# Performance work log

Measured on AMD Instinct MI355X. Metric: run time of the kernel, lower is better.

The kernel has to match this reference:

```python
import jax, jax.numpy as jnp
import numpy as np

B, L, D, H = 2, 2048, 1024, 16
DK = D // H
DFF = 4 * D
EPS = 1e-5  # torch LayerNorm default


def setup_inputs() -> dict:
    key = jax.random.key(0)
    ks = jax.random.split(key, 12)
    w = lambda k, shp: (jax.random.normal(k, shp, jnp.float32) * 0.02)
    return {
        "x": jax.random.normal(ks[0], (B, L, D), jnp.float32),
        "y": jax.random.normal(ks[1], (B, L, D), jnp.float32),
        "Wq": w(ks[2], (D, D)), "bq": jnp.zeros((D,), jnp.float32),
        "Wk": w(ks[3], (D, D)), "bk": jnp.zeros((D,), jnp.float32),
        "Wv": w(ks[4], (D, D)), "bv": jnp.zeros((D,), jnp.float32),
        "Wo": w(ks[5], (D, D)), "bo": jnp.zeros((D,), jnp.float32),
        "W1": w(ks[6], (D, DFF)), "b1": jnp.zeros((DFF,), jnp.float32),
        "W2": w(ks[7], (DFF, D)), "b2": jnp.zeros((D,), jnp.float32),
        "ln1_w": jnp.ones((L, D), jnp.float32), "ln1_b": jnp.zeros((L, D), jnp.float32),
        "ln2_w": jnp.ones((L, D), jnp.float32), "ln2_b": jnp.zeros((L, D), jnp.float32),
    }


def _layernorm2d(t, w, b):
    # nn.LayerNorm(normalized_shape=[L, D]): normalize jointly over last two dims
    mu = jnp.mean(t, axis=(-2, -1), keepdims=True)
    var = jnp.mean((t - mu) ** 2, axis=(-2, -1), keepdims=True)
    return (t - mu) * jax.lax.rsqrt(var + EPS) * w + b


def _attention(q_in, kv_in, Wq, bq, Wk, bk, Wv, bv, Wo, bo):
    split = lambda t: t.reshape(B, L, H, DK).transpose(0, 2, 1, 3)  # [B,H,L,DK]
    q = split(q_in @ Wq + bq)
    k = split(kv_in @ Wk + bk)
    v = split(kv_in @ Wv + bv)
    scores = jnp.einsum("bhqd,bhkd->bhqk", q, k) / (DK ** 0.5)
    # NOTE: original applies torch.tril to SCORES (zeroes upper triangle,
    # NOT -inf), so future positions still contribute exp(0)=1 in softmax.
    scores = jnp.tril(scores)
    p_attn = jax.nn.softmax(scores, axis=-1)
    out = jnp.einsum("bhqk,bhkd->bhqd", p_attn, v)
    out = out.transpose(0, 2, 1, 3).reshape(B, L, D)
    return out @ Wo + bo


def reference(x, y, Wq, bq, Wk, bk, Wv, bv, Wo, bo, W1, b1, W2, b2,
              ln1_w, ln1_b, ln2_w, ln2_b):
    # sublayer 0: pre-norm y, attention(query=x, key=value=norm(y)), residual
    y1 = y + _attention(x, _layernorm2d(y, ln1_w, ln1_b),
                        Wq, bq, Wk, bk, Wv, bv, Wo, bo)
    # sublayer 1: pre-norm, FFN (dropout inactive in eval), residual
    h = jax.nn.relu(_layernorm2d(y1, ln2_w, ln2_b) @ W1 + b1)
    return y1 + h @ W2 + b2
```

## Files before the change

### kernel.cpp

```cpp
#include <hip/hip_runtime.h>
#include <math.h>

#define B 2
#define L 2048
#define D 1024
#define H 16
#define DK 64
#define DFF 4096
#define EPS 1e-5f

typedef short short8 __attribute__((ext_vector_type(8)));
typedef short short4v __attribute__((ext_vector_type(4)));
typedef float float4v __attribute__((ext_vector_type(4)));
typedef unsigned int u32;

__device__ inline short f2bf(float f) {
    unsigned u = __builtin_bit_cast(unsigned, f);
    u += 0x7fffu + ((u >> 16) & 1u);
    return (short)(u >> 16);
}

__device__ inline float bf2f(short s) {
    unsigned u = ((unsigned)(unsigned short)s) << 16;
    return __builtin_bit_cast(float, u);
}

#define GLOAD_LDS16(gp, lp)                                                  \
    __builtin_amdgcn_global_load_lds(                                        \
        (const __attribute__((address_space(1))) u32*)(const void*)(gp),     \
        (__attribute__((address_space(3))) u32*)(void*)(lp), 16, 0, 0)

__device__ inline void xcd_remap(int& bx, int& by) {
    const int nbx = gridDim.x, nby = gridDim.y;
    const int orig = blockIdx.x + nbx * blockIdx.y;
    const int k = orig & 7, j = orig >> 3;
    const int nyc = nby >> 3;
    bx = j % nbx;
    by = k * nyc + j / nbx;
}


__global__ __launch_bounds__(256) void red_partial(const float* __restrict__ X,
                                                   float* __restrict__ part) {
    int b = blockIdx.y;
    const float4* p = (const float4*)(X + (size_t)b * L * D);
    float s = 0.f, ss = 0.f;
    for (int idx = blockIdx.x * 256 + threadIdx.x; idx < L * D / 4; idx += 256 * 256) {
        float4 v = p[idx];
        s += v.x + v.y + v.z + v.w;
        ss += v.x * v.x + v.y * v.y + v.z * v.z + v.w * v.w;
    }
    __shared__ float sh0[256], sh1[256];
    sh0[threadIdx.x] = s; sh1[threadIdx.x] = ss;
    __syncthreads();
    for (int o = 128; o; o >>= 1) {
        if (threadIdx.x < o) {
            sh0[threadIdx.x] += sh0[threadIdx.x + o];
            sh1[threadIdx.x] += sh1[threadIdx.x + o];
        }
        __syncthreads();
    }
    if (threadIdx.x == 0) {
        part[(b * 256 + blockIdx.x) * 2 + 0] = sh0[0];
        part[(b * 256 + blockIdx.x) * 2 + 1] = sh1[0];
    }
}

__global__ __launch_bounds__(256) void red_final(const float* __restrict__ part,
                                                 float* __restrict__ stats,
                                                 int npart) {
    int b = blockIdx.x;
    float s = 0.f, ss = 0.f;
    for (int i = threadIdx.x; i < npart; i += 256) {
        s += part[((size_t)b * npart + i) * 2 + 0];
        ss += part[((size_t)b * npart + i) * 2 + 1];
    }
    __shared__ float sh0[256], sh1[256];
    sh0[threadIdx.x] = s; sh1[threadIdx.x] = ss;
    __syncthreads();
    for (int o = 128; o; o >>= 1) {
        if (threadIdx.x < o) {
            sh0[threadIdx.x] += sh0[threadIdx.x + o];
            sh1[threadIdx.x] += sh1[threadIdx.x + o];
        }
        __syncthreads();
    }
    if (threadIdx.x == 0) {
        const float invN = 1.f / (float)(L * D);
        float mu = sh0[0] * invN;
        float var = sh1[0] * invN - mu * mu;
        stats[b * 2 + 0] = mu;
        stats[b * 2 + 1] = rsqrtf(var + EPS);
    }
}

__global__ __launch_bounds__(256) void ln_apply_bf(const float* __restrict__ X,
                                                   const float* __restrict__ W,
                                                   const float* __restrict__ Bb,
                                                   const float* __restrict__ stats,
                                                   short* __restrict__ Yn) {
    int b = blockIdx.y;
    float mu = stats[b * 2 + 0];
    float rstd = stats[b * 2 + 1];
    size_t e = (size_t)(blockIdx.x * 256 + threadIdx.x) * 4;
    const float4 xv = *(const float4*)(X + (size_t)b * L * D + e);
    const float4 wv = *(const float4*)(W + e);
    const float4 bv = *(const float4*)(Bb + e);
    short4v o;
    o[0] = f2bf((xv.x - mu) * rstd * wv.x + bv.x);
    o[1] = f2bf((xv.y - mu) * rstd * wv.y + bv.y);
    o[2] = f2bf((xv.z - mu) * rstd * wv.z + bv.z);
    o[3] = f2bf((xv.w - mu) * rstd * wv.w + bv.w);
    *(short4v*)(Yn + (size_t)b * L * D + e) = o;
}

__global__ __launch_bounds__(256) void convert_bf(const float* __restrict__ X,
                                                  short* __restrict__ Y) {
    size_t e = (size_t)(blockIdx.x * 256 + threadIdx.x) * 4;
    const float4 v = *(const float4*)(X + e);
    short4v o = {f2bf(v.x), f2bf(v.y), f2bf(v.z), f2bf(v.w)};
    *(short4v*)(Y + e) = o;
}

__global__ __launch_bounds__(256) void wt_transpose_all(
        const float* __restrict__ Wq, const float* __restrict__ Wk,
        const float* __restrict__ Wv, const float* __restrict__ Wo,
        const float* __restrict__ W1, const float* __restrict__ W2,
        short* __restrict__ WqT, short* __restrict__ WkvT,
        short* __restrict__ WoT, short* __restrict__ W1T,
        short* __restrict__ W2T) {
    const int id = blockIdx.x;
    const float* W; short* WT; int K, N, rel;
    if (id < 1024)      { W = Wq; WT = WqT;                    K = 1024; N = 1024; rel = id; }
    else if (id < 2048) { W = Wk; WT = WkvT;                   K = 1024; N = 1024; rel = id - 1024; }
    else if (id < 3072) { W = Wv; WT = WkvT + (size_t)D * D;   K = 1024; N = 1024; rel = id - 2048; }
    else if (id < 4096) { W = Wo; WT = WoT;                    K = 1024; N = 1024; rel = id - 3072; }
    else if (id < 8192) { W = W1; WT = W1T;                    K = 1024; N = 4096; rel = id - 4096; }
    else                { W = W2; WT = W2T;                    K = 4096; N = 1024; rel = id - 8192; }
    const int lb = (N == 4096) ? 7 : 5;
    const int bx = rel & ((1 << lb) - 1), by = rel >> lb;

    __shared__ short tile[32][33];
    const int t = threadIdx.x;
    const int tx = t & 31, ty = t >> 5;
    const int k0 = by * 32, n0 = bx * 32;
#pragma unroll
    for (int i = 0; i < 4; ++i) {
        const int k = ty + i * 8;
        tile[k][tx] = f2bf(W[(size_t)(k0 + k) * N + n0 + tx]);
    }
    __syncthreads();
#pragma unroll
    for (int i = 0; i < 4; ++i) {
        const int n = ty + i * 8;
        WT[(size_t)(n0 + n) * K + k0 + tx] = tile[tx][n];
    }
}


__device__ __forceinline__ void cv128_body(const short* __restrict__ A,
                                           const short* __restrict__ BT,
                                           const float* __restrict__ bias,
                                           const float* __restrict__ Res,
                                           void* __restrict__ Cout,
                                           int N, int Kloop, int lda, int flags,
                                           int m0, int n0,
                                           short* __restrict__ AsB,
                                           short* __restrict__ BsB) {
    const int t = threadIdx.x;
    const int wave = t >> 6, lane = t & 63;
    const int m16 = lane & 15, q4 = lane >> 4;
    const int wm = (wave >> 1) * 64, wn = (wave & 1) * 64;
    const int xorm = m16 & 7;
    const int BUFE = 128 * 64;

    float4v acc[4][4];
#pragma unroll
    for (int i = 0; i < 4; ++i)
#pragma unroll
        for (int j = 0; j < 4; ++j) acc[i][j] = (float4v){0.f, 0.f, 0.f, 0.f};

    auto stage = [&](int buf, int k0) {
        short* AsBuf = AsB + buf * BUFE;
        short* BsBuf = BsB + buf * BUFE;
#pragma unroll
        for (int p = 0; p < 4; ++p) {
            const int s = p * 256 + t;
            const int row = s >> 3;
            const int col = ((s & 7) ^ (row & 7)) * 8;
            GLOAD_LDS16(A + (size_t)(m0 + row) * lda + k0 + col,
                        AsBuf + (p * 256 + wave * 64) * 8);
        }
#pragma unroll
        for (int p = 0; p < 4; ++p) {
            const int s = p * 256 + t;
            const int row = s >> 3;
            const int col = ((s & 7) ^ (row & 7)) * 8;
            GLOAD_LDS16(BT + (size_t)(n0 + row) * lda + k0 + col,
                        BsBuf + (p * 256 + wave * 64) * 8);
        }
    };

    auto compute = [&](int buf) {
        const short* AsBuf = AsB + buf * BUFE;
        const short* BsBuf = BsB + buf * BUFE;
#pragma unroll
        for (int kk = 0; kk < 2; ++kk) {
            const int slot = ((kk * 4 + q4) ^ xorm) * 8;
            short8 af[4], bf[4];
#pragma unroll
            for (int mi = 0; mi < 4; ++mi)
                af[mi] = *(const short8*)&AsBuf[(wm + mi * 16 + m16) * 64 + slot];
#pragma unroll
            for (int ni = 0; ni < 4; ++ni)
                bf[ni] = *(const short8*)&BsBuf[(wn + ni * 16 + m16) * 64 + slot];
#pragma unroll
            for (int mi = 0; mi < 4; ++mi)
#pragma unroll
                for (int ni = 0; ni < 4; ++ni)
                    acc[mi][ni] = __builtin_amdgcn_mfma_f32_16x16x32_bf16(
                        af[mi], bf[ni], acc[mi][ni], 0, 0, 0);
        }
    };

    const int nt = Kloop >> 6;
    stage(0, 0);
    for (int ti = 0; ti < nt; ++ti) {
        const int cur = ti & 1;
        if (ti + 1 < nt) {
            stage(cur ^ 1, (ti + 1) << 6);
            asm volatile("s_waitcnt vmcnt(8)" ::: "memory");
        } else {
            asm volatile("s_waitcnt vmcnt(0)" ::: "memory");
        }
        __builtin_amdgcn_s_barrier();
        __builtin_amdgcn_sched_barrier(0);
        compute(cur);
        __builtin_amdgcn_s_barrier();
    }

#pragma unroll
    for (int mi = 0; mi < 4; ++mi)
#pragma unroll
        for (int ni = 0; ni < 4; ++ni) {
            const int col = n0 + wn + ni * 16 + m16;
            const float bb = bias ? bias[col] : 0.f;
#pragma unroll
            for (int r = 0; r < 4; ++r) {
                const int row = m0 + wm + mi * 16 + q4 * 4 + r;
                float v = acc[mi][ni][r] + bb;
                if (Res) v += Res[(size_t)row * N + col];
                if (flags & 1) v = fmaxf(v, 0.f);
                if (flags & 2)
                    ((short*)Cout)[(size_t)row * N + col] = f2bf(v);
                else
                    ((float*)Cout)[(size_t)row * N + col] = v;
            }
        }
}

__global__ __launch_bounds__(256) void gemm_qkv(const short* __restrict__ xb,
                                                const short* __restrict__ WqT,
                                                const float* __restrict__ bq,
                                                short* __restrict__ qb,
                                                const short* __restrict__ ynb,
                                                const short* __restrict__ WkvT,
                                                const float* __restrict__ bkv,
                                                short* __restrict__ kvb) {
    __shared__ short As[2][128 * 64];
    __shared__ short Bs[2][128 * 64];
    const int id = blockIdx.x;
    const int k = id & 7, j = id >> 3;
    const int lin = k * 96 + j;
    if (lin < 256) {
        const int bx = lin & 7, by = lin >> 3;
        cv128_body(xb, WqT, bq, nullptr, qb, 1024, 1024, 1024, 2,
                   by * 128, bx * 128, &As[0][0], &Bs[0][0]);
    } else {
        const int l2 = lin - 256;
        const int bx = l2 & 15, by = l2 >> 4;
        cv128_body(ynb, WkvT, bkv, nullptr, kvb, 2048, 1024, 1024, 2,
                   by * 128, bx * 128, &As[0][0], &Bs[0][0]);
    }
}

__global__ __launch_bounds__(256) void gemm_cv128_sk(const short* __restrict__ A,
                                                     const short* __restrict__ BT,
                                                     float* __restrict__ part,
                                                     int M, int N, int K) {
    __shared__ short As[2][128 * 64];
    __shared__ short Bs[2][128 * 64];
    const int id = blockIdx.x;
    const int k = id & 7, j = id >> 3;
    const int lin = k * 64 + j;
    const int ks = lin >> 8;
    const int rem = lin & 255;
    const int by = rem & 31, bx = (rem >> 5) & 7;
    const int Kc = K >> 1;
    cv128_body(A + ks * Kc, BT + ks * Kc, nullptr, nullptr,
               part + (size_t)ks * M * N, N, Kc, K, 0,
               by * 128, bx * 128, &As[0][0], &Bs[0][0]);
}

__global__ __launch_bounds__(256) void sk_reduce(const float* __restrict__ part,
                                                 const float* __restrict__ bias,
                                                 const float* __restrict__ Res,
                                                 float* __restrict__ out,
                                                 int MN, int N) {
    const size_t e = (size_t)(blockIdx.x * 256 + threadIdx.x) * 4;
    const float4 p0 = *(const float4*)(part + e);
    const float4 p1 = *(const float4*)(part + (size_t)MN + e);
    const float4 rv = *(const float4*)(Res + e);
    const float4 bv = *(const float4*)(bias + (e & (size_t)(N - 1)));
    float4 o;
    o.x = p0.x + p1.x + rv.x + bv.x;
    o.y = p0.y + p1.y + rv.y + bv.y;
    o.z = p0.z + p1.z + rv.z + bv.z;
    o.w = p0.w + p1.w + rv.w + bv.w;
    *(float4*)(out + e) = o;
}

__global__ __launch_bounds__(256) void sk_reduce_ln(const float* __restrict__ part,
                                                    const float* __restrict__ bias,
                                                    const float* __restrict__ Res,
                                                    float* __restrict__ out,
                                                    float* __restrict__ lnpart,
                                                    int MN) {
    const int b = blockIdx.y;
    const size_t e = ((size_t)b * 2048 + blockIdx.x) * 1024 + threadIdx.x * 4;
    const float4 p0 = *(const float4*)(part + e);
    const float4 p1 = *(const float4*)(part + (size_t)MN + e);
    const float4 rv = *(const float4*)(Res + e);
    const float4 bv = *(const float4*)(bias + threadIdx.x * 4);
    float4 o;
    o.x = p0.x + p1.x + rv.x + bv.x;
    o.y = p0.y + p1.y + rv.y + bv.y;
    o.z = p0.z + p1.z + rv.z + bv.z;
    o.w = p0.w + p1.w + rv.w + bv.w;
    *(float4*)(out + e) = o;
    float s = o.x + o.y + o.z + o.w;
    float ss = o.x * o.x + o.y * o.y + o.z * o.z + o.w * o.w;
    __shared__ float sh0[256], sh1[256];
    sh0[threadIdx.x] = s; sh1[threadIdx.x] = ss;
    __syncthreads();
    for (int off = 128; off; off >>= 1) {
        if (threadIdx.x < off) {
            sh0[threadIdx.x] += sh0[threadIdx.x + off];
            sh1[threadIdx.x] += sh1[threadIdx.x + off];
        }
        __syncthreads();
    }
    if (threadIdx.x == 0) {
        lnpart[((size_t)b * 2048 + blockIdx.x) * 2 + 0] = sh0[0];
        lnpart[((size_t)b * 2048 + blockIdx.x) * 2 + 1] = sh1[0];
    }
}

__global__ __launch_bounds__(512) void gemm_cv256(const short* __restrict__ A,
                                                  const short* __restrict__ BT,
                                                  const float* __restrict__ bias,
                                                  const float* __restrict__ Res,
                                                  void* __restrict__ Cout,
                                                  int M, int N, int K, int flags) {
    __shared__ short As[2][256 * 64];
    __shared__ short Bs[2][256 * 64];
    const int t = threadIdx.x;
    const int wave = t >> 6, lane = t & 63;
    const int m16 = lane & 15, q4 = lane >> 4;
    int bx, by;
    xcd_remap(bx, by);
    const int m0 = by * 256, n0 = bx * 256;
    const int wm = (wave >> 2) * 128, wn = (wave & 3) * 64;
    const int xorm = m16 & 7;

    float4v acc[8][4];
#pragma unroll
    for (int i = 0; i < 8; ++i)
#pragma unroll
        for (int j = 0; j < 4; ++j) acc[i][j] = (float4v){0.f, 0.f, 0.f, 0.f};

    auto stage = [&](int buf, int k0) {
#pragma unroll
        for (int p = 0; p < 4; ++p) {
            const int s = p * 512 + t;
            const int row = s >> 3;
            const int col = ((s & 7) ^ (row & 7)) * 8;
            short* lds = &As[buf][(p * 512 + wave * 64) * 8];
            GLOAD_LDS16(A + (size_t)(m0 + row) * K + k0 + col, lds);
        }
#pragma unroll
        for (int p = 0; p < 4; ++p) {
            const int s = p * 512 + t;
            const int row = s >> 3;
            const int col = ((s & 7) ^ (row & 7)) * 8;
            short* lds = &Bs[buf][(p * 512 + wave * 64) * 8];
            GLOAD_LDS16(BT + (size_t)(n0 + row) * K + k0 + col, lds);
        }
    };

    auto compute = [&](int buf) {
#pragma unroll
        for (int kk = 0; kk < 2; ++kk) {
            const int slot = ((kk * 4 + q4) ^ xorm) * 8;
            short8 af[8], bf[4];
#pragma unroll
            for (int mi = 0; mi < 8; ++mi)
                af[mi] = *(const short8*)&As[buf][(wm + mi * 16 + m16) * 64 + slot];
#pragma unroll
            for (int ni = 0; ni < 4; ++ni)
                bf[ni] = *(const short8*)&Bs[buf][(wn + ni * 16 + m16) * 64 + slot];
#pragma unroll
            for (int mi = 0; mi < 8; ++mi)
#pragma unroll
                for (int ni = 0; ni < 4; ++ni)
                    acc[mi][ni] = __builtin_amdgcn_mfma_f32_16x16x32_bf16(
                        af[mi], bf[ni], acc[mi][ni], 0, 0, 0);
        }
    };

    const int nt = K >> 6;
    stage(0, 0);
    for (int ti = 0; ti < nt; ++ti) {
        const int cur = ti & 1;
        if (ti + 1 < nt) {
            stage(cur ^ 1, (ti + 1) << 6);
            asm volatile("s_waitcnt vmcnt(8)" ::: "memory");
        } else {
            asm volatile("s_waitcnt vmcnt(0)" ::: "memory");
        }
        __builtin_amdgcn_s_barrier();
        __builtin_amdgcn_sched_barrier(0);
        compute(cur);
        __builtin_amdgcn_s_barrier();
    }

#pragma unroll
    for (int mi = 0; mi < 8; ++mi)
#pragma unroll
        for (int ni = 0; ni < 4; ++ni) {
            const int col = n0 + wn + ni * 16 + m16;
            const float bb = bias[col];
#pragma unroll
            for (int r = 0; r < 4; ++r) {
                const int row = m0 + wm + mi * 16 + q4 * 4 + r;
                float v = acc[mi][ni][r] + bb;
                if (Res) v += Res[(size_t)row * N + col];
                if (flags & 1) v = fmaxf(v, 0.f);
                if (flags & 2)
                    ((short*)Cout)[(size_t)row * N + col] = f2bf(v);
                else
                    ((float*)Cout)[(size_t)row * N + col] = v;
            }
        }
}


#define ASTR 72
#define SKV (2 * D)

__global__ __launch_bounds__(256) void v_transpose(const short* __restrict__ KVg,
                                                   short* __restrict__ VT,
                                                   float* __restrict__ Vtile) {
    __shared__ short tile[64 * ASTR];
    __shared__ float sh[4][64];
    const int t = threadIdx.x;
    const int bh = blockIdx.x >> 5;
    const int jt = blockIdx.x & 31;
    const int b = bh >> 4, h = bh & (H - 1);
    const size_t baseV = (size_t)b * L * SKV + (size_t)h * DK + D;
    const int j0 = jt * 64;
    const int sj = t >> 3, sd8 = (t & 7) * 8, sm = t & 7;
#pragma unroll
    for (int rep = 0; rep < 2; ++rep) {
        const int j = rep * 32 + sj;
        const short8 vv = *(const short8*)(KVg + baseV + (size_t)(j0 + j) * SKV + sd8);
        const int jsw = ((((j >> 3) ^ sm) << 3) | (j & 7));
#pragma unroll
        for (int i = 0; i < 8; ++i) tile[(sd8 + i) * ASTR + jsw] = vv[i];
    }
    __syncthreads();
#pragma unroll
    for (int rep = 0; rep < 2; ++rep) {
        const int s = rep * 256 + t;
        const int d = s >> 3, c = s & 7;
        const short8 vv = *(const short8*)&tile[d * ASTR + ((c ^ (d >> 3)) << 3)];
        *(short8*)(VT + ((size_t)bh * DK + d) * L + j0 + c * 8) = vv;
    }
    {
        const int d = t & 63, g = t >> 6;
        float s = 0.f;
#pragma unroll
        for (int c = 0; c < 16; ++c) s += bf2f(tile[d * ASTR + g * 16 + c]);
        sh[g][d] = s;
        __syncthreads();
        if (t < 64)
            Vtile[((size_t)bh * 32 + jt) * 64 + t] =
                sh[0][t] + sh[1][t] + sh[2][t] + sh[3][t];
    }
}

__global__ __launch_bounds__(64) void v_suffix(const float* __restrict__ Vtile,
                                               float* __restrict__ Vsuf) {
    const int bh = blockIdx.x;
    const int d = threadIdx.x;
    float s = 0.f;
    Vsuf[((size_t)bh * 33 + 32) * 64 + d] = 0.f;
    for (int kt = 31; kt >= 0; --kt) {
        s += Vtile[((size_t)bh * 32 + kt) * 64 + d];
        Vsuf[((size_t)bh * 33 + kt) * 64 + d] = s;
    }
}


__global__ __launch_bounds__(256) void attn_mfma(const short* __restrict__ Qg,
                                                 const short* __restrict__ KVg,
                                                 const short* __restrict__ VTg,
                                                 const float* __restrict__ Vsuf,
                                                 short* __restrict__ O) {
    __shared__ alignas(16) short Kb[2][64 * 64];
    __shared__ alignas(16) short Vt[2][64 * 64];
    __shared__ alignas(16) short Pb[64 * ASTR];

    const int t = threadIdx.x;
    const int wave = t >> 6;
    const int lane = t & 63;
    const int m16 = lane & 15;
    const int q4 = lane >> 4;

    const int u = blockIdx.x & 15;
    const int bh = blockIdx.x >> 4;
    const int h = bh & (H - 1);
    const int b = bh >> 4;
    const size_t baseQ = (size_t)b * L * D + (size_t)h * DK;
    const size_t baseK = (size_t)b * L * SKV + (size_t)h * DK;
    const size_t baseVT = (size_t)bh * DK * L;

    const int irow = wave * 16 + m16;
    const int ig = irow >> 3;
    const int xorm = m16 & 7;

    auto stage = [&](int buf, int kt0) {
#pragma unroll
        for (int rep = 0; rep < 2; ++rep) {
            const int s = rep * 256 + t;
            const int j = s >> 3;
            const int c = (s & 7) ^ (j & 7);
            GLOAD_LDS16(KVg + baseK + (size_t)(kt0 + j) * SKV + c * 8,
                        &Kb[buf][(rep * 256 + wave * 64) * 8]);
        }
#pragma unroll
        for (int rep = 0; rep < 2; ++rep) {
            const int s = rep * 256 + t;
            const int d = s >> 3;
            const int c = (s & 7) ^ (d & 7);
            GLOAD_LDS16(VTg + baseVT + (size_t)d * L + kt0 + c * 8,
                        &Vt[buf][(rep * 256 + wave * 64) * 8]);
        }
    };

#pragma unroll
    for (int pq = 0; pq < 2; ++pq) {
        const int qt = pq ? (31 - u) : u;
        const int q0 = qt * 64;
        const int rowA = q0 + wave * 16 + m16;

        short8 qf[2];
#pragma unroll
        for (int kc = 0; kc < 2; ++kc)
            qf[kc] = *(const short8*)(Qg + baseQ + (size_t)rowA * D + kc * 32 + q4 * 8);

        float lsum = 0.f;
        float4v acc[4];
#pragma unroll
        for (int f = 0; f < 4; ++f) acc[f] = (float4v){0.f, 0.f, 0.f, 0.f};

        stage(0, 0);
        for (int kt = 0; kt <= qt; ++kt) {
            const int cur = kt & 1;
            if (kt < qt) {
                stage(cur ^ 1, (kt + 1) * 64);
                asm volatile("s_waitcnt vmcnt(4)" ::: "memory");
            } else {
                asm volatile("s_waitcnt vmcnt(0)" ::: "memory");
            }
            __builtin_amdgcn_s_barrier();
            __builtin_amdgcn_sched_barrier(0);

            const short* KbC = &Kb[cur][0];
            const short* VtC = &Vt[cur][0];
            const bool diag = (kt == qt);

#pragma unroll
            for (int f = 0; f < 4; ++f) {
                const int krow = f * 16 + m16;
                const short8 kf0 = *(const short8*)&KbC[krow * 64 + ((q4 ^ xorm) << 3)];
                const short8 kf1 = *(const short8*)&KbC[krow * 64 + (((4 + q4) ^ xorm) << 3)];
                float4v sv = {0.f, 0.f, 0.f, 0.f};
                sv = __builtin_amdgcn_mfma_f32_16x16x32_bf16(kf0, qf[0], sv, 0, 0, 0);
                sv = __builtin_amdgcn_mfma_f32_16x16x32_bf16(kf1, qf[1], sv, 0, 0, 0);

                float pv[4];
                if (diag) {
#pragma unroll
                    for (int r = 0; r < 4; ++r) {
                        const int jl = f * 16 + q4 * 4 + r;
                        pv[r] = (jl <= irow) ? __expf(sv[r] * 0.125f) : 1.0f;
                    }
                } else {
#pragma unroll
                    for (int r = 0; r < 4; ++r) pv[r] = __expf(sv[r] * 0.125f);
                }
                lsum += pv[0] + pv[1] + pv[2] + pv[3];

                short4v s4;
                s4[0] = f2bf(pv[0]); s4[1] = f2bf(pv[1]);
                s4[2] = f2bf(pv[2]); s4[3] = f2bf(pv[3]);
                const int jb = f * 2 + (q4 >> 1);
                *(short4v*)&Pb[irow * ASTR + (((jb ^ ig) << 3) | ((q4 & 1) << 2))] = s4;
            }

#pragma unroll
            for (int kc = 0; kc < 2; ++kc) {
                const short8 pf = *(const short8*)&Pb[irow * ASTR + (((kc * 4 + q4) ^ ig) << 3)];
#pragma unroll
                for (int f = 0; f < 4; ++f) {
                    const int d = f * 16 + m16;
                    const short8 vf = *(const short8*)&VtC[d * 64 + (((kc * 4 + q4) ^ xorm) << 3)];
                    acc[f] = __builtin_amdgcn_mfma_f32_16x16x32_bf16(pf, vf, acc[f], 0, 0, 0);
                }
            }
            __builtin_amdgcn_s_barrier();
        }

        float s = lsum;
        s += __shfl_xor(s, 16);
        s += __shfl_xor(s, 32);
        s += (float)(L - (qt + 1) * 64);
        const float inv = 1.0f / s;
        float invr[4];
#pragma unroll
        for (int r = 0; r < 4; ++r) invr[r] = __shfl(inv, q4 * 4 + r);

        const float* vs = Vsuf + ((size_t)bh * 33 + qt + 1) * 64;
#pragma unroll
        for (int f = 0; f < 4; ++f) {
            const float vadd = vs[f * 16 + m16];
#pragma unroll
            for (int r = 0; r < 4; ++r) {
                const int i = q0 + wave * 16 + q4 * 4 + r;
                O[baseQ + (size_t)i * D + f * 16 + m16] = f2bf((acc[f][r] + vadd) * invr[r]);
            }
        }
    }
}


extern "C" void kernel_launch(void* const* d_in, const int* in_sizes, int n_in,
                              void* d_out, int out_size, void* d_ws, size_t ws_size,
                              hipStream_t stream) {
    const float* x    = (const float*)d_in[0];
    const float* y    = (const float*)d_in[1];
    const float* Wq   = (const float*)d_in[2];
    const float* bq   = (const float*)d_in[3];
    const float* Wk   = (const float*)d_in[4];
    const float* bk   = (const float*)d_in[5];
    const float* Wv   = (const float*)d_in[6];
    const float* bv   = (const float*)d_in[7];
    const float* Wo   = (const float*)d_in[8];
    const float* bo   = (const float*)d_in[9];
    const float* W1   = (const float*)d_in[10];
    const float* b1   = (const float*)d_in[11];
    const float* W2   = (const float*)d_in[12];
    const float* b2   = (const float*)d_in[13];
    const float* ln1w = (const float*)d_in[14];
    const float* ln1b = (const float*)d_in[15];
    const float* ln2w = (const float*)d_in[16];
    const float* ln2b = (const float*)d_in[17];
    float* out = (float*)d_out;

    const size_t F = (size_t)B * L * D;
    char* p = (char*)d_ws;
    short* xb    = (short*)p; p += F * 2;
    short* ynb   = (short*)p; p += F * 2;
    short* qb    = (short*)p; p += F * 2;
    short* kvb   = (short*)p; p += 2 * F * 2;
    short* aob   = (short*)p; p += F * 2;
    short* y1nb  = (short*)p; p += F * 2;
    short* hb    = (short*)p; p += (size_t)B * L * DFF * 2;
    float* y1    = (float*)p; p += F * 4;
    short* WqT   = (short*)p; p += (size_t)D * D * 2;
    short* WkvT  = (short*)p; p += (size_t)D * 2 * D * 2;
    short* WoT   = (short*)p; p += (size_t)D * D * 2;
    short* W1T   = (short*)p; p += (size_t)D * DFF * 2;
    short* W2T   = (short*)p; p += (size_t)D * DFF * 2;
    float* biaskv= (float*)p; p += 2 * D * 4;
    float* vtile = (float*)p; p += (size_t)B * H * 32 * DK * 4;
    float* vsuf  = (float*)p; p += (size_t)B * H * 33 * DK * 4;
    float* part  = (float*)p; p += (size_t)B * 2048 * 2 * 4;
    float* stats = (float*)p;

    short* vtb = hb;
    float* skpartWo = (float*)hb;
    float* skpart = (float*)qb;

    const int M = B * L;

    wt_transpose_all<<<dim3(12288), 256, 0, stream>>>(Wq, Wk, Wv, Wo, W1, W2,
                                                      WqT, WkvT, WoT, W1T, W2T);
    hipMemcpyAsync(biaskv,     bk, D * sizeof(float), hipMemcpyDeviceToDevice, stream);
    hipMemcpyAsync(biaskv + D, bv, D * sizeof(float), hipMemcpyDeviceToDevice, stream);

    convert_bf<<<dim3(F / 1024), 256, 0, stream>>>(x, xb);

    red_partial<<<dim3(256, B), 256, 0, stream>>>(y, part);
    red_final<<<dim3(B), 256, 0, stream>>>(part, stats, 256);
    ln_apply_bf<<<dim3(L * D / 1024, B), 256, 0, stream>>>(y, ln1w, ln1b, stats, ynb);

    gemm_qkv<<<dim3(768), 256, 0, stream>>>(xb, WqT, bq, qb, ynb, WkvT, biaskv, kvb);

    v_transpose<<<dim3(B * H * 32), 256, 0, stream>>>(kvb, vtb, vtile);
    v_suffix<<<dim3(B * H), 64, 0, stream>>>(vtile, vsuf);

    attn_mfma<<<dim3(B * H * 16), 256, 0, stream>>>(qb, kvb, vtb, vsuf, aob);

    gemm_cv128_sk<<<dim3(512), 256, 0, stream>>>(aob, WoT, skpartWo, M, D, D);
    sk_reduce_ln<<<dim3(2048, B), 256, 0, stream>>>(skpartWo, bo, y, y1, part, M * D);
    red_final<<<dim3(B), 256, 0, stream>>>(part, stats, 2048);
    ln_apply_bf<<<dim3(L * D / 1024, B), 256, 0, stream>>>(y1, ln2w, ln2b, stats, y1nb);

    gemm_cv256<<<dim3(DFF / 256, M / 256), 512, 0, stream>>>(y1nb, W1T, b1, nullptr, hb, M, DFF, D, 3);

    gemm_cv128_sk<<<dim3(512), 256, 0, stream>>>(hb, W2T, skpart, M, D, DFF);
    sk_reduce<<<dim3(M * D / 1024), 256, 0, stream>>>(skpart, b2, y1, out, M * D, D);
}
```

Baseline: 404.9 us.

## Merge prologue kernels and fold final reductions via last-block atomic counters

Weight transpose, x conversion, the LN1 partial reduction and the bias copy are merged into one prologue launch. The separate red_final and v_suffix launches are replaced by a last-block-done pattern using atomic counters and thread fences, with the counters zeroed by one memset. The softmax scale and log2(e) are folded into the Q projection epilogue so attention uses exp2f directly. This removes several kernel launches and per-score multiplies, at the cost of serial tail work in the last block and Q being stored pre-scaled in bf16.

Result: slower. 980.2 us (+142.1%).

```diff
diff --git a/kernel.cpp b/kernel.cpp
--- a/kernel.cpp
+++ b/kernel.cpp
@@ -8,6 +8,7 @@
 #define DK 64
 #define DFF 4096
 #define EPS 1e-5f
+#define QSCALE 0.18033688011112042f
 
 typedef short short8 __attribute__((ext_vector_type(8)));
 typedef short short4v __attribute__((ext_vector_type(4)));
@@ -40,57 +41,106 @@
 }
 
 
-__global__ __launch_bounds__(256) void red_partial(const float* __restrict__ X,
-                                                   float* __restrict__ part) {
-    int b = blockIdx.y;
-    const float4* p = (const float4*)(X + (size_t)b * L * D);
-    float s = 0.f, ss = 0.f;
-    for (int idx = blockIdx.x * 256 + threadIdx.x; idx < L * D / 4; idx += 256 * 256) {
-        float4 v = p[idx];
-        s += v.x + v.y + v.z + v.w;
-        ss += v.x * v.x + v.y * v.y + v.z * v.z + v.w * v.w;
-    }
-    __shared__ float sh0[256], sh1[256];
-    sh0[threadIdx.x] = s; sh1[threadIdx.x] = ss;
-    __syncthreads();
-    for (int o = 128; o; o >>= 1) {
-        if (threadIdx.x < o) {
-            sh0[threadIdx.x] += sh0[threadIdx.x + o];
-            sh1[threadIdx.x] += sh1[threadIdx.x + o];
+__global__ __launch_bounds__(256) void prologue(
+        const float* __restrict__ Wq, const float* __restrict__ Wk,
+        const float* __restrict__ Wv, const float* __restrict__ Wo,
+        const float* __restrict__ W1, const float* __restrict__ W2,
+        short* __restrict__ WqT, short* __restrict__ WkvT,
+        short* __restrict__ WoT, short* __restrict__ W1T,
+        short* __restrict__ W2T,
+        const float* __restrict__ x, short* __restrict__ xb,
+        const float* __restrict__ y, float* __restrict__ part,
+        float* __restrict__ stats,
+        const float* __restrict__ bk, const float* __restrict__ bv,
+        float* __restrict__ biaskv, int* __restrict__ ctr) {
+    const int id = blockIdx.x;
+    const int t = threadIdx.x;
+
+    if (id < 12288) {
+        const float* W; short* WT; int K, N, rel;
+        if (id < 1024)      { W = Wq; WT = WqT;                    K = 1024; N = 1024; rel = id; }
+        else if (id < 2048) { W = Wk; WT = WkvT;                   K = 1024; N = 1024; rel = id - 1024; }
+        else if (id < 3072) { W = Wv; WT = WkvT + (size_t)D * D;   K = 1024; N = 1024; rel = id - 2048; }
+        else if (id < 4096) { W = Wo; WT = WoT;                    K = 1024; N = 1024; rel = id - 3072; }
+        else if (id < 8192) { W = W1; WT = W1T;                    K = 1024; N = 4096; rel = id - 4096; }
+        else                { W = W2; WT = W2T;                    K = 4096; N = 1024; rel = id - 8192; }
+        const int lb = (N == 4096) ? 7 : 5;
+        const int bx = rel & ((1 << lb) - 1), by = rel >> lb;
+        __shared__ short tile[32][33];
+        const int tx = t & 31, ty = t >> 5;
+        const int k0 = by * 32, n0 = bx * 32;
+#pragma unroll
+        for (int i = 0; i < 4; ++i) {
+            const int k = ty + i * 8;
+            tile[k][tx] = f2bf(W[(size_t)(k0 + k) * N + n0 + tx]);
         }
         __syncthreads();
-    }
-    if (threadIdx.x == 0) {
-        part[(b * 256 + blockIdx.x) * 2 + 0] = sh0[0];
-        part[(b * 256 + blockIdx.x) * 2 + 1] = sh1[0];
-    }
-}
-
-__global__ __launch_bounds__(256) void red_final(const float* __restrict__ part,
-                                                 float* __restrict__ stats,
-                                                 int npart) {
-    int b = blockIdx.x;
-    float s = 0.f, ss = 0.f;
-    for (int i = threadIdx.x; i < npart; i += 256) {
-        s += part[((size_t)b * npart + i) * 2 + 0];
-        ss += part[((size_t)b * npart + i) * 2 + 1];
-    }
-    __shared__ float sh0[256], sh1[256];
-    sh0[threadIdx.x] = s; sh1[threadIdx.x] = ss;
-    __syncthreads();
-    for (int o = 128; o; o >>= 1) {
-        if (threadIdx.x < o) {
-            sh0[threadIdx.x] += sh0[threadIdx.x + o];
-            sh1[threadIdx.x] += sh1[threadIdx.x + o];
-        }
+#pragma unroll
+        for (int i = 0; i < 4; ++i) {
+            const int n = ty + i * 8;
+            WT[(size_t)(n0 + n) * K + k0 + tx] = tile[tx][n];
+        }
+        return;
+    }
+
+    if (id < 16384) {
+        const size_t e = ((size_t)(id - 12288) * 256 + t) * 4;
+        const float4 v = *(const float4*)(x + e);
+        short4v o = {f2bf(v.x), f2bf(v.y), f2bf(v.z), f2bf(v.w)};
+        *(short4v*)(xb + e) = o;
+        return;
+    }
+
+    if (id < 16896) {
+        const int rel = id - 16384;
+        const int b = rel >> 8, bx = rel & 255;
+        const float4* p = (const float4*)(y + (size_t)b * L * D);
+        float s = 0.f, ss = 0.f;
+        for (int idx = bx * 256 + t; idx < L * D / 4; idx += 256 * 256) {
+            float4 v = p[idx];
+            s += v.x + v.y + v.z + v.w;
+            ss += v.x * v.x + v.y * v.y + v.z * v.z + v.w * v.w;
+        }
+        __shared__ float sh0[256], sh1[256];
+        sh0[t] = s; sh1[t] = ss;
         __syncthreads();
-    }
-    if (threadIdx.x == 0) {
-        const float invN = 1.f / (float)(L * D);
-        float mu = sh0[0] * invN;
-        float var = sh1[0] * invN - mu * mu;
-        stats[b * 2 + 0] = mu;
-        stats[b * 2 + 1] = rsqrtf(var + EPS);
+        for (int o = 128; o; o >>= 1) {
+            if (t < o) { sh0[t] += sh0[t + o]; sh1[t] += sh1[t + o]; }
+            __syncthreads();
+        }
+        if (t == 0) {
+            part[(b * 256 + bx) * 2 + 0] = sh0[0];
+            part[(b * 256 + bx) * 2 + 1] = sh1[0];
+        }
+        __threadfence();
+        __shared__ int flag;
+        if (t == 0) flag = (atomicAdd(&ctr[b], 1) == 255);
+        __syncthreads();
+        if (flag) {
+            __threadfence();
+            float fs = part[(b * 256 + t) * 2 + 0];
+            float fss = part[(b * 256 + t) * 2 + 1];
+            __syncthreads();
+            sh0[t] = fs; sh1[t] = fss;
+            __syncthreads();
+            for (int o = 128; o; o >>= 1) {
+                if (t < o) { sh0[t] += sh0[t + o]; sh1[t] += sh1[t + o]; }
+                __syncthreads();
+            }
+            if (t == 0) {
+                const float invN = 1.f / (float)(L * D);
+                float mu = sh0[0] * invN;
+                float var = sh1[0] * invN - mu * mu;
+                stats[b * 2 + 0] = mu;
+                stats[b * 2 + 1] = rsqrtf(var + EPS);
+            }
+        }
+        return;
+    }
+
+    for (int i = t; i < D; i += 256) {
+        biaskv[i] = bk[i];
+        biaskv[D + i] = bv[i];
     }
 }
 
@@ -114,49 +164,6 @@
     *(short4v*)(Yn + (size_t)b * L * D + e) = o;
 }
 
-__global__ __launch_bounds__(256) void convert_bf(const float* __restrict__ X,
-                                                  short* __restrict__ Y) {
-    size_t e = (size_t)(blockIdx.x * 256 + threadIdx.x) * 4;
-    const float4 v = *(const float4*)(X + e);
-    short4v o = {f2bf(v.x), f2bf(v.y), f2bf(v.z), f2bf(v.w)};
-    *(short4v*)(Y + e) = o;
-}
-
-__global__ __launch_bounds__(256) void wt_transpose_all(
-        const float* __restrict__ Wq, const float* __restrict__ Wk,
-        const float* __restrict__ Wv, const float* __restrict__ Wo,
-        const float* __restrict__ W1, const float* __restrict__ W2,
-        short* __restrict__ WqT, short* __restrict__ WkvT,
-        short* __restrict__ WoT, short* __restrict__ W1T,
-        short* __restrict__ W2T) {
-    const int id = blockIdx.x;
-    const float* W; short* WT; int K, N, rel;
-    if (id < 1024)      { W = Wq; WT = WqT;                    K = 1024; N = 1024; rel = id; }
-    else if (id < 2048) { W = Wk; WT = WkvT;                   K = 1024; N = 1024; rel = id - 1024; }
-    else if (id < 3072) { W = Wv; WT = WkvT + (size_t)D * D;   K = 1024; N = 1024; rel = id - 2048; }
-    else if (id < 4096) { W = Wo; WT = WoT;                    K = 1024; N = 1024; rel = id - 3072; }
-    else if (id < 8192) { W = W1; WT = W1T;                    K = 1024; N = 4096; rel = id - 4096; }
-    else                { W = W2; WT = W2T;                    K = 4096; N = 1024; rel = id - 8192; }
-    const int lb = (N == 4096) ? 7 : 5;
-    const int bx = rel & ((1 << lb) - 1), by = rel >> lb;
-
-    __shared__ short tile[32][33];
-    const int t = threadIdx.x;
-    const int tx = t & 31, ty = t >> 5;
-    const int k0 = by * 32, n0 = bx * 32;
-#pragma unroll
-    for (int i = 0; i < 4; ++i) {
-        const int k = ty + i * 8;
-        tile[k][tx] = f2bf(W[(size_t)(k0 + k) * N + n0 + tx]);
-    }
-    __syncthreads();
-#pragma unroll
-    for (int i = 0; i < 4; ++i) {
-        const int n = ty + i * 8;
-        WT[(size_t)(n0 + n) * K + k0 + tx] = tile[tx][n];
-    }
-}
-
 
 __device__ __forceinline__ void cv128_body(const short* __restrict__ A,
                                            const short* __restrict__ BT,
@@ -251,6 +258,7 @@
                 float v = acc[mi][ni][r] + bb;
                 if (Res) v += Res[(size_t)row * N + col];
                 if (flags & 1) v = fmaxf(v, 0.f);
+                if (flags & 4) v *= QSCALE;
                 if (flags & 2)
                     ((short*)Cout)[(size_t)row * N + col] = f2bf(v);
                 else
@@ -274,7 +282,7 @@
     const int lin = k * 96 + j;
     if (lin < 256) {
         const int bx = lin & 7, by = lin >> 3;
-        cv128_body(xb, WqT, bq, nullptr, qb, 1024, 1024, 1024, 2,
+        cv128_body(xb, WqT, bq, nullptr, qb, 1024, 1024, 1024, 2 | 4,
                    by * 128, bx * 128, &As[0][0], &Bs[0][0]);
     } else {
         const int l2 = lin - 256;
@@ -325,13 +333,16 @@
                                                     const float* __restrict__ Res,
                                                     float* __restrict__ out,
                                                     float* __restrict__ lnpart,
+                                                    float* __restrict__ stats,
+                                                    int* __restrict__ ctr,
                                                     int MN) {
     const int b = blockIdx.y;
-    const size_t e = ((size_t)b * 2048 + blockIdx.x) * 1024 + threadIdx.x * 4;
+    const int t = threadIdx.x;
+    const size_t e = ((size_t)b * 2048 + blockIdx.x) * 1024 + t * 4;
     const float4 p0 = *(const float4*)(part + e);
     const float4 p1 = *(const float4*)(part + (size_t)MN + e);
     const float4 rv = *(const float4*)(Res + e);
-    const float4 bv = *(const float4*)(bias + threadIdx.x * 4);
+    const float4 bv = *(const float4*)(bias + t * 4);
     float4 o;
     o.x = p0.x + p1.x + rv.x + bv.x;
     o.y = p0.y + p1.y + rv.y + bv.y;
@@ -341,18 +352,41 @@
     float s = o.x + o.y + o.z + o.w;
     float ss = o.x * o.x + o.y * o.y + o.z * o.z + o.w * o.w;
     __shared__ float sh0[256], sh1[256];
-    sh0[threadIdx.x] = s; sh1[threadIdx.x] = ss;
+    sh0[t] = s; sh1[t] = ss;
     __syncthreads();
     for (int off = 128; off; off >>= 1) {
-        if (threadIdx.x < off) {
-            sh0[threadIdx.x] += sh0[threadIdx.x + off];
-            sh1[threadIdx.x] += sh1[threadIdx.x + off];
-        }
+        if (t < off) { sh0[t] += sh0[t + off]; sh1[t] += sh1[t + off]; }
         __syncthreads();
     }
-    if (threadIdx.x == 0) {
+    if (t == 0) {
         lnpart[((size_t)b * 2048 + blockIdx.x) * 2 + 0] = sh0[0];
         lnpart[((size_t)b * 2048 + blockIdx.x) * 2 + 1] = sh1[0];
+    }
+    __threadfence();
+    __shared__ int flag;
+    if (t == 0) flag = (atomicAdd(&ctr[b], 1) == 2047);
+    __syncthreads();
+    if (flag) {
+        __threadfence();
+        float fs = 0.f, fss = 0.f;
+        for (int i = t; i < 2048; i += 256) {
+            fs += lnpart[((size_t)b * 2048 + i) * 2 + 0];
+            fss += lnpart[((size_t)b * 2048 + i) * 2 + 1];
+        }
+        __syncthreads();
+        sh0[t] = fs; sh1[t] = fss;
+        __syncthreads();
+        for (int off = 128; off; off >>= 1) {
+            if (t < off) { sh0[t] += sh0[t + off]; sh1[t] += sh1[t + off]; }
+            __syncthreads();
+        }
+        if (t == 0) {
+            const float invN = 1.f / (float)(L * D);
+            float mu = sh0[0] * invN;
+            float var = sh1[0] * invN - mu * mu;
+            stats[b * 2 + 0] = mu;
+            stats[b * 2 + 1] = rsqrtf(var + EPS);
+        }
     }
 }
 
@@ -460,7 +494,9 @@
 
 __global__ __launch_bounds__(256) void v_transpose(const short* __restrict__ KVg,
                                                    short* __restrict__ VT,
-                                                   float* __restrict__ Vtile) {
+                                                   float* __restrict__ Vtile,
+                                                   float* __restrict__ Vsuf,
+                                                   int* __restrict__ ctr) {
     __shared__ short tile[64 * ASTR];
     __shared__ float sh[4][64];
     const int t = threadIdx.x;
@@ -497,17 +533,20 @@
             Vtile[((size_t)bh * 32 + jt) * 64 + t] =
                 sh[0][t] + sh[1][t] + sh[2][t] + sh[3][t];
     }
-}
-
-__global__ __launch_bounds__(64) void v_suffix(const float* __restrict__ Vtile,
-                                               float* __restrict__ Vsuf) {
-    const int bh = blockIdx.x;
-    const int d = threadIdx.x;
-    float s = 0.f;
-    Vsuf[((size_t)bh * 33 + 32) * 64 + d] = 0.f;
-    for (int kt = 31; kt >= 0; --kt) {
-        s += Vtile[((size_t)bh * 32 + kt) * 64 + d];
-        Vsuf[((size_t)bh * 33 + kt) * 64 + d] = s;
+    __threadfence();
+    __shared__ int flag;
+    if (t == 0) flag = (atomicAdd(&ctr[bh], 1) == 31);
+    __syncthreads();
+    if (flag) {
+        __threadfence();
+        if (t < 64) {
+            float s = 0.f;
+            Vsuf[((size_t)bh * 33 + 32) * 64 + t] = 0.f;
+            for (int kt = 31; kt >= 0; --kt) {
+                s += Vtile[((size_t)bh * 32 + kt) * 64 + t];
+                Vsuf[((size_t)bh * 33 + kt) * 64 + t] = s;
+            }
+        }
     }
 }
 
@@ -604,11 +643,11 @@
 #pragma unroll
                     for (int r = 0; r < 4; ++r) {
                         const int jl = f * 16 + q4 * 4 + r;
-                        pv[r] = (jl <= irow) ? __expf(sv[r] * 0.125f) : 1.0f;
+                        pv[r] = (jl <= irow) ? exp2f(sv[r]) : 1.0f;
                     }
                 } else {
 #pragma unroll
-                    for (int r = 0; r < 4; ++r) pv[r] = __expf(sv[r] * 0.125f);
+                    for (int r = 0; r < 4; ++r) pv[r] = exp2f(sv[r]);
                 }
                 lsum += pv[0] + pv[1] + pv[2] + pv[3];
 
@@ -697,7 +736,8 @@
     float* vtile = (float*)p; p += (size_t)B * H * 32 * DK * 4;
     float* vsuf  = (float*)p; p += (size_t)B * H * 33 * DK * 4;
     float* part  = (float*)p; p += (size_t)B * 2048 * 2 * 4;
-    float* stats = (float*)p;
+    float* stats = (float*)p; p += 4 * 4;
+    int*   ctrs  = (int*)p;   p += 64 * 4;
 
     short* vtb = hb;
     float* skpartWo = (float*)hb;
@@ -705,27 +745,24 @@
 
     const int M = B * L;
 
-    wt_transpose_all<<<dim3(12288), 256, 0, stream>>>(Wq, Wk, Wv, Wo, W1, W2,
-                                                      WqT, WkvT, WoT, W1T, W2T);
-    hipMemcpyAsync(biaskv,     bk, D * sizeof(float), hipMemcpyDeviceToDevice, stream);
-    hipMemcpyAsync(biaskv + D, bv, D * sizeof(float), hipMemcpyDeviceToDevice, stream);
-
-    convert_bf<<<dim3(F / 1024), 256, 0, stream>>>(x, xb);
-
-    red_partial<<<dim3(256, B), 256, 0, stream>>>(y, part);
-    red_final<<<dim3(B), 256, 0, stream>>>(part, stats, 256);
+    hipMemsetAsync(ctrs, 0, 64 * sizeof(int), stream);
+
+    prologue<<<dim3(16897), 256, 0, stream>>>(Wq, Wk, Wv, Wo, W1, W2,
+                                              WqT, WkvT, WoT, W1T, W2T,
+                                              x, xb, y, part, stats,
+                                              bk, bv, biaskv, ctrs);
+
     ln_apply_bf<<<dim3(L * D / 1024, B), 256, 0, stream>>>(y, ln1w, ln1b, stats, ynb);
 
     gemm_qkv<<<dim3(768), 256, 0, stream>>>(xb, WqT, bq, qb, ynb, WkvT, biaskv, kvb);
 
-    v_transpose<<<dim3(B * H * 32), 256, 0, stream>>>(kvb, vtb, vtile);
-    v_suffix<<<dim3(B * H), 64, 0, stream>>>(vtile, vsuf);
+    v_transpose<<<dim3(B * H * 32), 256, 0, stream>>>(kvb, vtb, vtile, vsuf, ctrs + 2);
 
     attn_mfma<<<dim3(B * H * 16), 256, 0, stream>>>(qb, kvb, vtb, vsuf, aob);
 
     gemm_cv128_sk<<<dim3(512), 256, 0, stream>>>(aob, WoT, skpartWo, M, D, D);
-    sk_reduce_ln<<<dim3(2048, B), 256, 0, stream>>>(skpartWo, bo, y, y1, part, M * D);
-    red_final<<<dim3(B), 256, 0, stream>>>(part, stats, 2048);
+    sk_reduce_ln<<<dim3(2048, B), 256, 0, stream>>>(skpartWo, bo, y, y1, part,
+                                                    stats, ctrs + 34, M * D);
     ln_apply_bf<<<dim3(L * D / 1024, B), 256, 0, stream>>>(y1, ln2w, ln2b, stats, y1nb);
 
     gemm_cv256<<<dim3(DFF / 256, M / 256), 512, 0, stream>>>(y1nb, W1T, b1, nullptr, hb, M, DFF, D, 3);
```
